# Kernel optimization log

Hardware: AMD Instinct MI355X
Metric: run time of the kernel (lower is better)

## Reference

```python
import jax, jax.numpy as jnp
import numpy as np
import math


def _proj(x, W, b):
    # 1x1 conv: x [B,C,H,W], W [O,C], b [O]
    return jnp.einsum('bchw,oc->bohw', x, W) + b[None, :, None, None]


def _head(x, Win, bin_, Wh, bh, Wout, bout):
    # in-layer ProjConv (no skip) with ReLU
    h = jax.nn.relu(_proj(x, Win, bin_))
    # hidden ProjConv layers with skip connection (kernel_size == 1 branch)
    for i in range(Wh.shape[0]):  # static small layer count
        h = h + jax.nn.relu(_proj(h, Wh[i], bh[i]))
    # out-layer ProjConv (logits, no activation)
    return _proj(h, Wout, bout)


def _forward(x, cls_Win, cls_bin, cls_Wh, cls_bh, cls_Wout, cls_bout,
             obj_Win, obj_bin, obj_Wh, obj_bh, obj_Wout, obj_bout,
             box_Win, box_bin, box_Wh, box_bh, box_Wout, box_bout,
             pos_Win, pos_bin, pos_Wh, pos_bh, pos_Wout, pos_bout,
             ins_Win, ins_bin, ins_Wh, ins_bh, ins_Wout, ins_bout):
    cls_logits = _head(x, cls_Win, cls_bin, cls_Wh, cls_bh, cls_Wout, cls_bout)  # [B,81,H,W]
    obj_logits = _head(x, obj_Win, obj_bin, obj_Wh, obj_bh, obj_Wout, obj_bout)  # [B,2,H,W]
    box_logits = _head(x, box_Win, box_bin, box_Wh, box_bh, box_Wout, box_bout)  # [B,4,H,W]
    pos_feats = _head(x, pos_Win, pos_bin, pos_Wh, pos_bh, pos_Wout, pos_bout)   # [B,64,H,W]
    ins_feats = _head(x, ins_Win, ins_bin, ins_Wh, ins_bh, ins_Wout, ins_bout)   # [B,128,H,W]
    return jnp.concatenate([cls_logits, obj_logits, box_logits, pos_feats, ins_feats], axis=1)


def setup_inputs() -> dict:
    key = jax.random.key(0)
    ks = iter(jax.random.split(key, 64))
    F, Cin, L = 64, 64, 2
    d = {'x': jax.random.normal(next(ks), (4, Cin, 256, 256), dtype=jnp.float32)}
    outs = {'cls': 81, 'obj': 2, 'box': 4, 'pos': 64, 'ins': 128}
    prior_bias = -math.log((1.0 - 0.01) / 0.01)  # prior_prob init for cls/obj out biases
    bias0 = {'cls': prior_bias, 'obj': prior_bias, 'box': 0.0, 'pos': 0.0, 'ins': 0.0}
    for name, od in outs.items():
        d[name + '_Win'] = (jax.random.normal(next(ks), (F, Cin)) * 0.05).astype(jnp.float32)
        d[name + '_bin'] = jnp.zeros((F,), dtype=jnp.float32)
        d[name + '_Wh'] = (jax.random.normal(next(ks), (L, F, F)) * 0.05).astype(jnp.float32)
        d[name + '_bh'] = jnp.zeros((L, F), dtype=jnp.float32)
        d[name + '_Wout'] = (jax.random.normal(next(ks), (od, F)) * 0.05).astype(jnp.float32)
        d[name + '_bout'] = jnp.full((od,), bias0[name], dtype=jnp.float32)
    return d


def reference(x, cls_Win, cls_bin, cls_Wh, cls_bh, cls_Wout, cls_bout,
              obj_Win, obj_bin, obj_Wh, obj_bh, obj_Wout, obj_bout,
              box_Win, box_bin, box_Wh, box_bh, box_Wout, box_bout,
              pos_Win, pos_bin, pos_Wh, pos_bh, pos_Wout, pos_bout,
              ins_Win, ins_bin, ins_Wh, ins_bh, ins_Wout, ins_bout):
    return _forward(x, cls_Win, cls_bin, cls_Wh, cls_bh, cls_Wout, cls_bout,
                    obj_Win, obj_bin, obj_Wh, obj_bh, obj_Wout, obj_bout,
                    box_Win, box_bin, box_Wh, box_bh, box_Wout, box_bout,
                    pos_Win, pos_bin, pos_Wh, pos_bh, pos_Wout, pos_bout,
                    ins_Win, ins_bin, ins_Wh, ins_bh, ins_Wout, ins_bout)
```

## Files before the change

### kernel.cpp

```cpp
#include <hip/hip_runtime.h>

typedef unsigned short u16;
typedef unsigned int   u32;
typedef __attribute__((ext_vector_type(8)))  short bf16x8;
typedef __attribute__((ext_vector_type(16))) float f32x16;

constexpr int NPIX = 4 * 65536;

__device__ constexpr int OD_[5]   = {81, 2, 4, 64, 128};
__device__ constexpr int NFO_[5]  = {3, 1, 1, 2, 4};
__device__ constexpr int COFF_[5] = {0, 81, 83, 87, 151};
__device__ constexpr int FB_[5]   = {0, 36, 64, 92, 124};

struct PW { const float* w[20]; };
struct PB {
    const float* x; float* out; const u16* wf;
    const float* b[20];
};

__device__ __forceinline__ void f2bf(float v, u16& h, u16& l) {
    u32 bi = __builtin_bit_cast(u32, v);
    u32 bh = bi & 0xffff0000u;
    h = (u16)(bi >> 16);
    float vl = v - __builtin_bit_cast(float, bh);
    l = (u16)(__builtin_bit_cast(u32, vl) >> 16);
}

__global__ __launch_bounds__(256) void prep_weights(PW wp, u16* wf) {
    int slot = blockIdx.x * 256 + threadIdx.x;
    if (slot >= 164 * 64) return;
    int frag = slot >> 6, lane = slot & 63;
    int fb = 0, seg = 0;
    for (int s = 0; s < 20; ++s) {
        int h = s >> 2, ly = s & 3;
        int cnt = (ly < 3) ? 8 : 4 * NFO_[h];
        if (frag < fb + cnt) { seg = s; break; }
        fb += cnt;
    }
    int h = seg >> 2, ly = seg & 3;
    int lf = frag - fb;
    int nf = lf >> 2, ks = lf & 3;
    int col  = nf * 32 + (lane & 31);
    int ksrc = ks * 16 + (lane >> 5) * 8;
    int rows = (ly < 3) ? 64 : OD_[h];
    const float* W = wp.w[seg];
    float wv[8];
    if (col < rows) {
        const float4* q = reinterpret_cast<const float4*>(W + col * 64 + ksrc);
        float4 a = q[0], c = q[1];
        wv[0]=a.x; wv[1]=a.y; wv[2]=a.z; wv[3]=a.w;
        wv[4]=c.x; wv[5]=c.y; wv[6]=c.z; wv[7]=c.w;
    } else {
#pragma unroll
        for (int j = 0; j < 8; ++j) wv[j] = 0.f;
    }
    bf16x8 vh, vl;
#pragma unroll
    for (int j = 0; j < 8; ++j) {
        u16 hh, ll; f2bf(wv[j], hh, ll);
        vh[j] = (short)hh; vl[j] = (short)ll;
    }
    u16* dst = wf + (size_t)frag * 1024 + lane * 8;
    *(bf16x8*)dst         = vh;
    *(bf16x8*)(dst + 512) = vl;
}

__device__ __forceinline__ u32 swz(int row, int ch) {
    return (u32)((row << 7) + (ch << 1)) ^ (u32)((row & 7) << 4);
}

template<bool SKIP>
__device__ __forceinline__ void run_layer(const u16* sh, const u16* sl,
                                          u16* dh, u16* dl,
                                          const u16* wf, int fb,
                                          const float* bias, int l) {
    int arow = l & 31, hb = (l >> 5) * 8;
    bf16x8 Ah[4], Al[4];
#pragma unroll
    for (int ks = 0; ks < 4; ++ks) {
        u32 off = swz(arow, ks * 16 + hb);
        Ah[ks] = *(const bf16x8*)((const char*)sh + off);
        Al[ks] = *(const bf16x8*)((const char*)sl + off);
    }
    bf16x8 Bh[2][4], Bl[2][4];
#pragma unroll
    for (int nf = 0; nf < 2; ++nf)
#pragma unroll
        for (int ks = 0; ks < 4; ++ks) {
            const u16* f = wf + (size_t)(fb + nf * 4 + ks) * 1024 + l * 8;
            Bh[nf][ks] = *(const bf16x8*)f;
            Bl[nf][ks] = *(const bf16x8*)(f + 512);
        }
#pragma unroll
    for (int nf = 0; nf < 2; ++nf) {
        int ch = nf * 32 + (l & 31);
        float bv = bias[ch];
        f32x16 acc;
#pragma unroll
        for (int i = 0; i < 16; ++i) acc[i] = 0.f;
#pragma unroll
        for (int ks = 0; ks < 4; ++ks) {
            acc = __builtin_amdgcn_mfma_f32_32x32x16_bf16(Ah[ks], Bh[nf][ks], acc, 0, 0, 0);
            acc = __builtin_amdgcn_mfma_f32_32x32x16_bf16(Ah[ks], Bl[nf][ks], acc, 0, 0, 0);
            acc = __builtin_amdgcn_mfma_f32_32x32x16_bf16(Al[ks], Bh[nf][ks], acc, 0, 0, 0);
        }
#pragma unroll
        for (int reg = 0; reg < 16; ++reg) {
            int row = (reg & 3) + 8 * (reg >> 2) + 4 * (l >> 5);
            float v = acc[reg] + bv;
            v = fmaxf(v, 0.f);
            u32 off = swz(row, ch);
            if (SKIP) {
                u16 oh = *(const u16*)((const char*)dh + off);
                u16 ol = *(const u16*)((const char*)dl + off);
                v += __builtin_bit_cast(float, (u32)oh << 16)
                   + __builtin_bit_cast(float, (u32)ol << 16);
            }
            u16 nh, nl; f2bf(v, nh, nl);
            *(u16*)((char*)dh + off) = nh;
            *(u16*)((char*)dl + off) = nl;
        }
    }
}

__device__ __forceinline__ void run_out(const u16* sh, const u16* sl,
                                        const u16* wf, int fb,
                                        const float* bout, int od, int nfo,
                                        float* out, size_t cb, int l) {
    int arow = l & 31, hb = (l >> 5) * 8;
    bf16x8 Ah[4], Al[4];
#pragma unroll
    for (int ks = 0; ks < 4; ++ks) {
        u32 off = swz(arow, ks * 16 + hb);
        Ah[ks] = *(const bf16x8*)((const char*)sh + off);
        Al[ks] = *(const bf16x8*)((const char*)sl + off);
    }
    for (int nf = 0; nf < nfo; ++nf) {
        bf16x8 Bh[4], Bl[4];
#pragma unroll
        for (int ks = 0; ks < 4; ++ks) {
            const u16* f = wf + (size_t)(fb + nf * 4 + ks) * 1024 + l * 8;
            Bh[ks] = *(const bf16x8*)f;
            Bl[ks] = *(const bf16x8*)(f + 512);
        }
        int col = nf * 32 + (l & 31);
        float bv = (col < od) ? bout[col] : 0.f;
        f32x16 acc;
#pragma unroll
        for (int i = 0; i < 16; ++i) acc[i] = 0.f;
#pragma unroll
        for (int ks = 0; ks < 4; ++ks) {
            acc = __builtin_amdgcn_mfma_f32_32x32x16_bf16(Ah[ks], Bh[ks], acc, 0, 0, 0);
            acc = __builtin_amdgcn_mfma_f32_32x32x16_bf16(Ah[ks], Bl[ks], acc, 0, 0, 0);
            acc = __builtin_amdgcn_mfma_f32_32x32x16_bf16(Al[ks], Bh[ks], acc, 0, 0, 0);
        }
        if (col < od) {
            float* op = out + cb + ((size_t)col << 16);
#pragma unroll
            for (int reg = 0; reg < 16; ++reg) {
                int row = (reg & 3) + 8 * (reg >> 2) + 4 * (l >> 5);
                op[row] = acc[reg] + bv;
            }
        }
    }
}

__global__ __launch_bounds__(256) void heads_main(PB p) {
    __shared__ u16 lds[4][4][2048];
    int tid = threadIdx.x;
    int w = tid >> 6, l = tid & 63;
    u16* Xh = lds[w][0]; u16* Xl = lds[w][1];
    u16* Hh = lds[w][2]; u16* Hl = lds[w][3];

    int p0  = blockIdx.x * 128 + w * 32;
    int b   = p0 >> 16, hw0 = p0 & 65535;
    const float* xb = p.x + ((size_t)(b * 64) << 16) + hw0;

#pragma unroll
    for (int i = 0; i < 8; ++i) {
        int c  = i * 8 + (l >> 3);
        int pq = (l & 7) * 4;
        float4 v4 = *reinterpret_cast<const float4*>(xb + ((size_t)c << 16) + pq);
        float tmp[4] = {v4.x, v4.y, v4.z, v4.w};
#pragma unroll
        for (int q = 0; q < 4; ++q) {
            int row = pq + q;
            u16 hh, ll; f2bf(tmp[q], hh, ll);
            u32 off = swz(row, c);
            *(u16*)((char*)Xh + off) = hh;
            *(u16*)((char*)Xl + off) = ll;
        }
    }
    asm volatile("" ::: "memory");

    for (int h = 0; h < 5; ++h) {
        int fb = FB_[h];
        run_layer<false>(Xh, Xl, Hh, Hl, p.wf, fb,      p.b[4*h],     l);
        asm volatile("" ::: "memory");
        run_layer<true >(Hh, Hl, Hh, Hl, p.wf, fb + 8,  p.b[4*h + 1], l);
        asm volatile("" ::: "memory");
        run_layer<true >(Hh, Hl, Hh, Hl, p.wf, fb + 16, p.b[4*h + 2], l);
        asm volatile("" ::: "memory");
        size_t cb = ((size_t)(b * 279 + COFF_[h]) << 16) + (size_t)hw0;
        run_out(Hh, Hl, p.wf, fb + 24, p.b[4*h + 3], OD_[h], NFO_[h], p.out, cb, l);
        asm volatile("" ::: "memory");
    }
}

extern "C" void kernel_launch(void* const* d_in, const int* in_sizes, int n_in,
                              void* d_out, int out_size, void* d_ws, size_t ws_size,
                              hipStream_t stream)
{
    auto A = [&](int i) { return (const float*)d_in[i]; };
    PW wp; PB pb;
    for (int h = 0; h < 5; ++h) {
        const float* Win  = A(1 + 6*h + 0);
        const float* bin  = A(1 + 6*h + 1);
        const float* Wh   = A(1 + 6*h + 2);
        const float* bh   = A(1 + 6*h + 3);
        const float* Wout = A(1 + 6*h + 4);
        const float* bout = A(1 + 6*h + 5);
        wp.w[4*h+0] = Win;  wp.w[4*h+1] = Wh;  wp.w[4*h+2] = Wh + 4096; wp.w[4*h+3] = Wout;
        pb.b[4*h+0] = bin;  pb.b[4*h+1] = bh;  pb.b[4*h+2] = bh + 64;   pb.b[4*h+3] = bout;
    }
    u16* wf = (u16*)d_ws;
    pb.x = (const float*)d_in[0];
    pb.out = (float*)d_out;
    pb.wf = wf;

    prep_weights<<<41, 256, 0, stream>>>(wp, wf);
    heads_main<<<NPIX / 128, 256, 0, stream>>>(pb);
}
```

Measured before the change: 561.9 us.

## Keep input fragments in registers and store hidden activations as fp32 in LDS

The input tile is now loaded straight from global memory into register-resident split-bf16 A fragments, with no LDS staging, and reused across all five heads. Hidden activations are kept in LDS as fp32 and split into hi/lo bf16 only when read back as A operands, so the skip add needs one float read instead of two u16 reads. The two output-column MFMA chains are interleaved per k-step with weights loaded just in time, output stores are vectorised to float4, and launch bounds request 4 blocks per CU. In exchange, each hidden layer load now does the split arithmetic, and the strided scalar global loads of x may coalesce less well than the old float4 loads.

```diff
diff --git a/kernel.cpp b/kernel.cpp
--- a/kernel.cpp
+++ b/kernel.cpp
@@ -3,6 +3,7 @@
 typedef unsigned short u16;
 typedef unsigned int   u32;
 typedef __attribute__((ext_vector_type(8)))  short bf16x8;
+typedef __attribute__((ext_vector_type(4)))  float f32x4;
 typedef __attribute__((ext_vector_type(16))) float f32x16;
 
 constexpr int NPIX = 4 * 65536;
@@ -13,17 +14,13 @@
 __device__ constexpr int FB_[5]   = {0, 36, 64, 92, 124};
 
 struct PW { const float* w[20]; };
-struct PB {
-    const float* x; float* out; const u16* wf;
-    const float* b[20];
-};
-
-__device__ __forceinline__ void f2bf(float v, u16& h, u16& l) {
+struct PB { const float* x; float* out; const u16* wf; const float* b[20]; };
+
+__device__ __forceinline__ void split2(float v, short& hi, short& lo) {
     u32 bi = __builtin_bit_cast(u32, v);
-    u32 bh = bi & 0xffff0000u;
-    h = (u16)(bi >> 16);
-    float vl = v - __builtin_bit_cast(float, bh);
-    l = (u16)(__builtin_bit_cast(u32, vl) >> 16);
+    float lof = v - __builtin_bit_cast(float, bi & 0xffff0000u);
+    hi = (short)(bi >> 16);
+    lo = (short)(__builtin_bit_cast(u32, lof) >> 16);
 }
 
 __global__ __launch_bounds__(256) void prep_weights(PW wp, u16* wf) {
@@ -56,153 +53,131 @@
     }
     bf16x8 vh, vl;
 #pragma unroll
-    for (int j = 0; j < 8; ++j) {
-        u16 hh, ll; f2bf(wv[j], hh, ll);
-        vh[j] = (short)hh; vl[j] = (short)ll;
-    }
+    for (int j = 0; j < 8; ++j) { short a, b; split2(wv[j], a, b); vh[j]=a; vl[j]=b; }
     u16* dst = wf + (size_t)frag * 1024 + lane * 8;
     *(bf16x8*)dst         = vh;
     *(bf16x8*)(dst + 512) = vl;
 }
 
-__device__ __forceinline__ u32 swz(int row, int ch) {
-    return (u32)((row << 7) + (ch << 1)) ^ (u32)((row & 7) << 4);
-}
-
-template<bool SKIP>
-__device__ __forceinline__ void run_layer(const u16* sh, const u16* sl,
-                                          u16* dh, u16* dl,
-                                          const u16* wf, int fb,
-                                          const float* bias, int l) {
-    int arow = l & 31, hb = (l >> 5) * 8;
-    bf16x8 Ah[4], Al[4];
+__device__ __forceinline__ u32 hswz(int row, int ch) {
+    return (u32)((row << 8) + (ch << 2)) ^ (u32)((row & 7) << 4);
+}
+
+__device__ __forceinline__ void load_a(const char* H, int arow, int ks, int hb,
+                                       bf16x8& ah, bf16x8& al) {
+    u32 o0 = hswz(arow, ks * 16 + hb);
+    f32x4 q0 = *(const f32x4*)(H + o0);
+    f32x4 q1 = *(const f32x4*)(H + (o0 ^ 16));
+    float qa[8] = {q0.x, q0.y, q0.z, q0.w, q1.x, q1.y, q1.z, q1.w};
+#pragma unroll
+    for (int j = 0; j < 8; ++j) { short a, b; split2(qa[j], a, b); ah[j]=a; al[j]=b; }
+}
+
+template<bool SKIP, bool FROM_LDS>
+__device__ __forceinline__ void proj_layer(const bf16x8* Xh, const bf16x8* Xl,
+                                           char* H, const u16* wfb,
+                                           const float* bias, int l) {
+    int hb = (l >> 5) * 8, arow = l & 31, hi4 = (l >> 5) * 4;
+    f32x16 acc0, acc1;
+#pragma unroll
+    for (int i = 0; i < 16; ++i) { acc0[i] = 0.f; acc1[i] = 0.f; }
 #pragma unroll
     for (int ks = 0; ks < 4; ++ks) {
-        u32 off = swz(arow, ks * 16 + hb);
-        Ah[ks] = *(const bf16x8*)((const char*)sh + off);
-        Al[ks] = *(const bf16x8*)((const char*)sl + off);
-    }
-    bf16x8 Bh[2][4], Bl[2][4];
-#pragma unroll
-    for (int nf = 0; nf < 2; ++nf)
-#pragma unroll
-        for (int ks = 0; ks < 4; ++ks) {
-            const u16* f = wf + (size_t)(fb + nf * 4 + ks) * 1024 + l * 8;
-            Bh[nf][ks] = *(const bf16x8*)f;
-            Bl[nf][ks] = *(const bf16x8*)(f + 512);
-        }
-#pragma unroll
-    for (int nf = 0; nf < 2; ++nf) {
+        bf16x8 ah, al;
+        if (FROM_LDS) load_a(H, arow, ks, hb, ah, al);
+        else          { ah = Xh[ks]; al = Xl[ks]; }
+        const u16* f0 = wfb + (size_t)ks * 1024;
+        const u16* f1 = wfb + (size_t)(4 + ks) * 1024;
+        bf16x8 b0h = *(const bf16x8*)f0, b0l = *(const bf16x8*)(f0 + 512);
+        bf16x8 b1h = *(const bf16x8*)f1, b1l = *(const bf16x8*)(f1 + 512);
+        acc0 = __builtin_amdgcn_mfma_f32_32x32x16_bf16(ah, b0h, acc0, 0, 0, 0);
+        acc0 = __builtin_amdgcn_mfma_f32_32x32x16_bf16(ah, b0l, acc0, 0, 0, 0);
+        acc0 = __builtin_amdgcn_mfma_f32_32x32x16_bf16(al, b0h, acc0, 0, 0, 0);
+        acc1 = __builtin_amdgcn_mfma_f32_32x32x16_bf16(ah, b1h, acc1, 0, 0, 0);
+        acc1 = __builtin_amdgcn_mfma_f32_32x32x16_bf16(ah, b1l, acc1, 0, 0, 0);
+        acc1 = __builtin_amdgcn_mfma_f32_32x32x16_bf16(al, b1h, acc1, 0, 0, 0);
+    }
+    auto epi = [&](const f32x16& acc, int nf) {
         int ch = nf * 32 + (l & 31);
         float bv = bias[ch];
+#pragma unroll
+        for (int reg = 0; reg < 16; ++reg) {
+            int row = (reg & 3) + 8 * (reg >> 2) + hi4;
+            u32 off = hswz(row, ch);
+            float v = fmaxf(acc[reg] + bv, 0.f);
+            if (SKIP) v += *(const float*)(H + off);
+            *(float*)(H + off) = v;
+        }
+    };
+    epi(acc0, 0);
+    epi(acc1, 1);
+}
+
+__device__ __forceinline__ void out_layer(const char* H, const u16* wfb,
+                                          const float* bout, int od, int nfo,
+                                          float* op_base, int l) {
+    int hb = (l >> 5) * 8, arow = l & 31, hi4 = (l >> 5) * 4;
+    bf16x8 Ah[4], Al[4];
+#pragma unroll
+    for (int ks = 0; ks < 4; ++ks) load_a(H, arow, ks, hb, Ah[ks], Al[ks]);
+    for (int nf = 0; nf < nfo; ++nf) {
         f32x16 acc;
 #pragma unroll
         for (int i = 0; i < 16; ++i) acc[i] = 0.f;
 #pragma unroll
         for (int ks = 0; ks < 4; ++ks) {
-            acc = __builtin_amdgcn_mfma_f32_32x32x16_bf16(Ah[ks], Bh[nf][ks], acc, 0, 0, 0);
-            acc = __builtin_amdgcn_mfma_f32_32x32x16_bf16(Ah[ks], Bl[nf][ks], acc, 0, 0, 0);
-            acc = __builtin_amdgcn_mfma_f32_32x32x16_bf16(Al[ks], Bh[nf][ks], acc, 0, 0, 0);
-        }
-#pragma unroll
-        for (int reg = 0; reg < 16; ++reg) {
-            int row = (reg & 3) + 8 * (reg >> 2) + 4 * (l >> 5);
-            float v = acc[reg] + bv;
-            v = fmaxf(v, 0.f);
-            u32 off = swz(row, ch);
-            if (SKIP) {
-                u16 oh = *(const u16*)((const char*)dh + off);
-                u16 ol = *(const u16*)((const char*)dl + off);
-                v += __builtin_bit_cast(float, (u32)oh << 16)
-                   + __builtin_bit_cast(float, (u32)ol << 16);
+            const u16* f = wfb + (size_t)(nf * 4 + ks) * 1024;
+            bf16x8 bh = *(const bf16x8*)f, bl = *(const bf16x8*)(f + 512);
+            acc = __builtin_amdgcn_mfma_f32_32x32x16_bf16(Ah[ks], bh, acc, 0, 0, 0);
+            acc = __builtin_amdgcn_mfma_f32_32x32x16_bf16(Ah[ks], bl, acc, 0, 0, 0);
+            acc = __builtin_amdgcn_mfma_f32_32x32x16_bf16(Al[ks], bh, acc, 0, 0, 0);
+        }
+        int col = nf * 32 + (l & 31);
+        if (col < od) {
+            float bv = bout[col];
+            float* op = op_base + ((size_t)col << 16);
+#pragma unroll
+            for (int g = 0; g < 4; ++g) {
+                int r0 = 8 * g + hi4;
+                f32x4 st = {acc[4*g+0] + bv, acc[4*g+1] + bv,
+                            acc[4*g+2] + bv, acc[4*g+3] + bv};
+                *(f32x4*)(op + r0) = st;
             }
-            u16 nh, nl; f2bf(v, nh, nl);
-            *(u16*)((char*)dh + off) = nh;
-            *(u16*)((char*)dl + off) = nl;
-        }
-    }
-}
-
-__device__ __forceinline__ void run_out(const u16* sh, const u16* sl,
-                                        const u16* wf, int fb,
-                                        const float* bout, int od, int nfo,
-                                        float* out, size_t cb, int l) {
-    int arow = l & 31, hb = (l >> 5) * 8;
-    bf16x8 Ah[4], Al[4];
-#pragma unroll
-    for (int ks = 0; ks < 4; ++ks) {
-        u32 off = swz(arow, ks * 16 + hb);
-        Ah[ks] = *(const bf16x8*)((const char*)sh + off);
-        Al[ks] = *(const bf16x8*)((const char*)sl + off);
-    }
-    for (int nf = 0; nf < nfo; ++nf) {
-        bf16x8 Bh[4], Bl[4];
-#pragma unroll
-        for (int ks = 0; ks < 4; ++ks) {
-            const u16* f = wf + (size_t)(fb + nf * 4 + ks) * 1024 + l * 8;
-            Bh[ks] = *(const bf16x8*)f;
-            Bl[ks] = *(const bf16x8*)(f + 512);
-        }
-        int col = nf * 32 + (l & 31);
-        float bv = (col < od) ? bout[col] : 0.f;
-        f32x16 acc;
-#pragma unroll
-        for (int i = 0; i < 16; ++i) acc[i] = 0.f;
-#pragma unroll
-        for (int ks = 0; ks < 4; ++ks) {
-            acc = __builtin_amdgcn_mfma_f32_32x32x16_bf16(Ah[ks], Bh[ks], acc, 0, 0, 0);
-            acc = __builtin_amdgcn_mfma_f32_32x32x16_bf16(Ah[ks], Bl[ks], acc, 0, 0, 0);
-            acc = __builtin_amdgcn_mfma_f32_32x32x16_bf16(Al[ks], Bh[ks], acc, 0, 0, 0);
-        }
-        if (col < od) {
-            float* op = out + cb + ((size_t)col << 16);
-#pragma unroll
-            for (int reg = 0; reg < 16; ++reg) {
-                int row = (reg & 3) + 8 * (reg >> 2) + 4 * (l >> 5);
-                op[row] = acc[reg] + bv;
-            }
-        }
-    }
-}
-
-__global__ __launch_bounds__(256) void heads_main(PB p) {
-    __shared__ u16 lds[4][4][2048];
-    int tid = threadIdx.x;
-    int w = tid >> 6, l = tid & 63;
-    u16* Xh = lds[w][0]; u16* Xl = lds[w][1];
-    u16* Hh = lds[w][2]; u16* Hl = lds[w][3];
-
-    int p0  = blockIdx.x * 128 + w * 32;
-    int b   = p0 >> 16, hw0 = p0 & 65535;
-    const float* xb = p.x + ((size_t)(b * 64) << 16) + hw0;
-
-#pragma unroll
-    for (int i = 0; i < 8; ++i) {
-        int c  = i * 8 + (l >> 3);
-        int pq = (l & 7) * 4;
-        float4 v4 = *reinterpret_cast<const float4*>(xb + ((size_t)c << 16) + pq);
-        float tmp[4] = {v4.x, v4.y, v4.z, v4.w};
-#pragma unroll
-        for (int q = 0; q < 4; ++q) {
-            int row = pq + q;
-            u16 hh, ll; f2bf(tmp[q], hh, ll);
-            u32 off = swz(row, c);
-            *(u16*)((char*)Xh + off) = hh;
-            *(u16*)((char*)Xl + off) = ll;
-        }
-    }
-    asm volatile("" ::: "memory");
-
+        }
+    }
+}
+
+__global__ __launch_bounds__(256, 4) void heads_main(PB p) {
+    __shared__ char Hs[4][8192];
+    int tid = threadIdx.x, w = tid >> 6, l = tid & 63;
+    char* H = Hs[w];
+    int p0 = blockIdx.x * 128 + w * 32;
+    int b = p0 >> 16, hw0 = p0 & 65535;
+    int hb = (l >> 5) * 8;
+    const float* xb = p.x + ((size_t)(b * 64) << 16) + hw0 + (l & 31);
+
+    bf16x8 Xh[4], Xl[4];
+#pragma unroll
+    for (int ks = 0; ks < 4; ++ks)
+#pragma unroll
+        for (int j = 0; j < 8; ++j) {
+            int ch = ks * 16 + hb + j;
+            float v = xb[(size_t)ch << 16];
+            short a, c; split2(v, a, c);
+            Xh[ks][j] = a; Xl[ks][j] = c;
+        }
+
+    const u16* wfl = p.wf + l * 8;
     for (int h = 0; h < 5; ++h) {
-        int fb = FB_[h];
-        run_layer<false>(Xh, Xl, Hh, Hl, p.wf, fb,      p.b[4*h],     l);
-        asm volatile("" ::: "memory");
-        run_layer<true >(Hh, Hl, Hh, Hl, p.wf, fb + 8,  p.b[4*h + 1], l);
-        asm volatile("" ::: "memory");
-        run_layer<true >(Hh, Hl, Hh, Hl, p.wf, fb + 16, p.b[4*h + 2], l);
-        asm volatile("" ::: "memory");
-        size_t cb = ((size_t)(b * 279 + COFF_[h]) << 16) + (size_t)hw0;
-        run_out(Hh, Hl, p.wf, fb + 24, p.b[4*h + 3], OD_[h], NFO_[h], p.out, cb, l);
+        const u16* wfb = wfl + (size_t)FB_[h] * 1024;
+        proj_layer<false, false>(Xh, Xl, H, wfb,              p.b[4*h+0], l);
+        asm volatile("" ::: "memory");
+        proj_layer<true,  true >(Xh, Xl, H, wfb +  8 * 1024,  p.b[4*h+1], l);
+        asm volatile("" ::: "memory");
+        proj_layer<true,  true >(Xh, Xl, H, wfb + 16 * 1024,  p.b[4*h+2], l);
+        asm volatile("" ::: "memory");
+        float* op = p.out + ((size_t)(b * 279 + COFF_[h]) << 16) + hw0;
+        out_layer(H, wfb + 24 * 1024, p.b[4*h+3], OD_[h], NFO_[h], op, l);
         asm volatile("" ::: "memory");
     }
 }
@@ -214,14 +189,14 @@
     auto A = [&](int i) { return (const float*)d_in[i]; };
     PW wp; PB pb;
     for (int h = 0; h < 5; ++h) {
-        const float* Win  = A(1 + 6*h + 0);
-        const float* bin  = A(1 + 6*h + 1);
-        const float* Wh   = A(1 + 6*h + 2);
-        const float* bh   = A(1 + 6*h + 3);
-        const float* Wout = A(1 + 6*h + 4);
-        const float* bout = A(1 + 6*h + 5);
-        wp.w[4*h+0] = Win;  wp.w[4*h+1] = Wh;  wp.w[4*h+2] = Wh + 4096; wp.w[4*h+3] = Wout;
-        pb.b[4*h+0] = bin;  pb.b[4*h+1] = bh;  pb.b[4*h+2] = bh + 64;   pb.b[4*h+3] = bout;
+        wp.w[4*h+0] = A(1 + 6*h + 0);
+        wp.w[4*h+1] = A(1 + 6*h + 2);
+        wp.w[4*h+2] = A(1 + 6*h + 2) + 4096;
+        wp.w[4*h+3] = A(1 + 6*h + 4);
+        pb.b[4*h+0] = A(1 + 6*h + 1);
+        pb.b[4*h+1] = A(1 + 6*h + 3);
+        pb.b[4*h+2] = A(1 + 6*h + 3) + 64;
+        pb.b[4*h+3] = A(1 + 6*h + 5);
     }
     u16* wf = (u16*)d_ws;
     pb.x = (const float*)d_in[0];
```

After: 560.3 us. About the same (-0.3%).
